# Performance work log

Measured on AMD Instinct MI355X. Metric: run time of the kernel, lower is better.

The kernel has to match this reference:

```python
import jax, jax.numpy as jnp
import numpy as np

B, N, M, D = 1, 16384, 16384, 3
CHUNK = 2048          # x tile size for the online-min KNN pass
NN_WEIGHT = 1.0       # self.nn_weight
# both_ways=False, free_weight=0, ch_normals_K=0 -> only cham_x branch is active


def setup_inputs() -> dict:
    key = jax.random.key(0)
    k1, k2, k3 = jax.random.split(key, 3)
    # LiDAR-like point clouds, scaled to a ~20 m scene extent
    pc1 = jax.random.normal(k1, (B, N, D), dtype=jnp.float32) * 10.0
    est_flow = jax.random.normal(k2, (B, N, D), dtype=jnp.float32) * 0.1
    pc2 = jax.random.normal(k3, (B, M, D), dtype=jnp.float32) * 10.0
    return {"pc1": pc1, "est_flow": est_flow, "pc2": pc2}


def _knn1_l1_dists(x, y):
    """Per-point min L1 distance from x [N,3] to y [M,3], tiled over x.

    Equivalent to knn_points(x, y, K=1, norm=1).dists[..., 0] without
    materializing the full [N, M] distance matrix.
    """
    n = x.shape[0]
    x_tiles = x.reshape(n // CHUNK, CHUNK, D)

    def tile_min(xc):  # xc: [CHUNK, 3]
        d = jnp.sum(jnp.abs(xc[:, None, :] - y[None, :, :]), axis=-1)  # [CHUNK, M]
        return jnp.min(d, axis=-1)                                     # [CHUNK]

    return jax.lax.map(tile_min, x_tiles).reshape(n)


def reference(pc1, est_flow, pc2):
    x = pc1 + est_flow                                   # deformed cloud [B,N,3]
    cham_x = jax.vmap(_knn1_l1_dists)(x, pc2)            # [B, N]
    cham_y = jnp.float32(0.0)                            # both_ways=False
    freespace_loss = jnp.zeros_like(cham_x)              # free_weight == 0 branch
    chamf_loss = NN_WEIGHT * (cham_x.mean() + cham_y)    # free_weight * 0 omitted
    return (chamf_loss, freespace_loss)
```

## Files before the change

kernel.cpp:

```cpp
#include <hip/hip_runtime.h>


#define TPB 256
#define RB 8
#define PTS_PER_BLOCK (TPB * RB)
#define YSEG 64
#define NITER (YSEG / 16)

typedef float sf16 __attribute__((ext_vector_type(16)));
typedef float sf8  __attribute__((ext_vector_type(8)));

#define SLOAD24(B16, B8, PTR, O16, O8)                                     \
  asm volatile("s_load_dwordx16 %0, %2, " O16 "\n\t"                       \
               "s_load_dwordx8  %1, %2, " O8                               \
               : "=s"(B16), "=s"(B8) : "s"(PTR));

#define SWAIT(B16, B8)                                                     \
  asm volatile("s_waitcnt lgkmcnt(0)" : "+s"(B16), "+s"(B8));

#define DIST2S(MR, AXv, AYv, AZv, Y0X, Y0Y, Y0Z, Y1X, Y1Y, Y1Z)           \
  {                                                                        \
    float t0, t1, t2, t3, t4;                                              \
    asm("v_sub_f32 %1, %9, %6\n\t"                                         \
        "v_sub_f32 %2, %10, %7\n\t"                                        \
        "v_sub_f32 %3, %11, %8\n\t"                                        \
        "v_sub_f32 %4, %12, %6\n\t"                                        \
        "v_sub_f32 %5, %13, %7\n\t"                                        \
        "v_add_f32 %1, |%1|, |%2|\n\t"                                     \
        "v_sub_f32 %2, %14, %8\n\t"                                        \
        "v_add_f32 %4, |%4|, |%5|\n\t"                                     \
        "v_add_f32 %1, %1, |%3|\n\t"                                       \
        "v_add_f32 %4, %4, |%2|\n\t"                                       \
        "v_min3_f32 %0, %0, %1, %4"                                        \
        : "+v"(MR), "=&v"(t0), "=&v"(t1), "=&v"(t2), "=&v"(t3), "=&v"(t4)  \
        : "v"(AXv), "v"(AYv), "v"(AZv),                                    \
          "s"(Y0X), "s"(Y0Y), "s"(Y0Z), "s"(Y1X), "s"(Y1Y), "s"(Y1Z));    \
  }

#define COMPUTE8(G16, G8)                                                  \
  {                                                                        \
    _Pragma("unroll")                                                      \
    for (int r = 0; r < RB; ++r)                                           \
      DIST2S(m[r], ax[r], ay[r], az[r],                                    \
             G16[0], G16[1], G16[2], G16[3], G16[4], G16[5]);              \
    _Pragma("unroll")                                                      \
    for (int r = 0; r < RB; ++r)                                           \
      DIST2S(m[r], ax[r], ay[r], az[r],                                    \
             G16[6], G16[7], G16[8], G16[9], G16[10], G16[11]);            \
    _Pragma("unroll")                                                      \
    for (int r = 0; r < RB; ++r)                                           \
      DIST2S(m[r], ax[r], ay[r], az[r],                                    \
             G16[12], G16[13], G16[14], G16[15], G8[0], G8[1]);            \
    _Pragma("unroll")                                                      \
    for (int r = 0; r < RB; ++r)                                           \
      DIST2S(m[r], ax[r], ay[r], az[r],                                    \
             G8[2], G8[3], G8[4], G8[5], G8[6], G8[7]);                    \
  }

__global__ __launch_bounds__(TPB) void init_kernel(unsigned* __restrict__ minbits, int N4) {
    const int i = blockIdx.x * TPB + threadIdx.x;
    uint4* p = (uint4*)minbits;
    if (i < N4) p[i] = make_uint4(0x7F7F7F7Fu, 0x7F7F7F7Fu, 0x7F7F7F7Fu, 0x7F7F7F7Fu);
}

__global__ __launch_bounds__(TPB, 8) void chamfer_kernel(
    const float* __restrict__ pc1, const float* __restrict__ flow,
    const float* __restrict__ pc2, unsigned* __restrict__ minbits,
    int N, int M) {
    const int t = threadIdx.x;

    const int ibase = blockIdx.x * PTS_PER_BLOCK + t;
    float ax[RB], ay[RB], az[RB];
#pragma unroll
    for (int r = 0; r < RB; ++r) {
        const int i = ibase + r * TPB;
        const int ic = (i < N) ? i : (N - 1);
        ax[r] = pc1[3 * ic]     + flow[3 * ic];
        ay[r] = pc1[3 * ic + 1] + flow[3 * ic + 1];
        az[r] = pc1[3 * ic + 2] + flow[3 * ic + 2];
    }

    float m[RB];
#pragma unroll
    for (int r = 0; r < RB; ++r) m[r] = 3.0e38f;

    const int ybase = blockIdx.y * YSEG;
    const int yend  = (ybase + YSEG < M) ? (ybase + YSEG) : M;

    if (yend - ybase == YSEG) {
        const float* yp = pc2 + (size_t)3 * (size_t)ybase;
        sf16 A16, B16; sf8 A8, B8;
        SLOAD24(A16, A8, yp, "0", "64");
#pragma unroll 1
        for (int it = 0; it < NITER; ++it) {
            SWAIT(A16, A8);
            SLOAD24(B16, B8, yp, "96", "160");
            COMPUTE8(A16, A8);
            SWAIT(B16, B8);
            if (it + 1 < NITER)
                SLOAD24(A16, A8, yp, "192", "256");
            COMPUTE8(B16, B8);
            yp += 48;
        }
    } else {
        for (int j = ybase; j < yend; ++j) {
            const float yx = pc2[3 * j], yy = pc2[3 * j + 1], yz = pc2[3 * j + 2];
#pragma unroll
            for (int r = 0; r < RB; ++r)
                m[r] = fminf(m[r], fabsf(ax[r] - yx) + fabsf(ay[r] - yy) + fabsf(az[r] - yz));
        }
    }

#pragma unroll
    for (int r = 0; r < RB; ++r) {
        const int i = ibase + r * TPB;
        if (i < N) atomicMin(&minbits[i], __float_as_uint(m[r]));
    }
}

__global__ __launch_bounds__(1024) void reduce_kernel(
    const unsigned* __restrict__ minbits, float* __restrict__ out,
    int N, int out_size) {
    float4* o4 = (float4*)out;
    const int n4 = out_size / 4;
    for (int k = threadIdx.x; k < n4; k += 1024)
        o4[k] = make_float4(0.f, 0.f, 0.f, 0.f);
    for (int k = n4 * 4 + threadIdx.x; k < out_size; k += 1024)
        out[k] = 0.f;

    float s = 0.0f;
    const uint4* p = (const uint4*)minbits;
    for (int k = threadIdx.x; k < N / 4; k += 1024) {
        uint4 v = p[k];
        s += __uint_as_float(v.x) + __uint_as_float(v.y) +
             __uint_as_float(v.z) + __uint_as_float(v.w);
    }
    for (int k = (N / 4) * 4 + threadIdx.x; k < N; k += 1024)
        s += __uint_as_float(minbits[k]);
#pragma unroll
    for (int off = 32; off > 0; off >>= 1) s += __shfl_down(s, off, 64);
    __shared__ float ls[16];
    const int wid = threadIdx.x >> 6, lane = threadIdx.x & 63;
    if (lane == 0) ls[wid] = s;
    __syncthreads();
    if (threadIdx.x == 0) {
        float tot = 0.0f;
        for (int w = 0; w < 16; ++w) tot += ls[w];
        out[0] = tot / (float)N;
    }
}

extern "C" void kernel_launch(void* const* d_in, const int* in_sizes, int n_in,
                              void* d_out, int out_size, void* d_ws, size_t ws_size,
                              hipStream_t stream) {
    const float* pc1  = (const float*)d_in[0];
    const float* flow = (const float*)d_in[1];
    const float* pc2  = (const float*)d_in[2];
    float* out = (float*)d_out;

    const int N = in_sizes[0] / 3;
    const int M = in_sizes[2] / 3;

    unsigned* minbits = (unsigned*)d_ws;

    const int nbN    = (N + PTS_PER_BLOCK - 1) / PTS_PER_BLOCK;
    const int msplit = (M + YSEG - 1) / YSEG;

    init_kernel<<<(N / 4 + TPB - 1) / TPB, TPB, 0, stream>>>(minbits, N / 4);
    chamfer_kernel<<<dim3(nbN, msplit), TPB, 0, stream>>>(pc1, flow, pc2, minbits, N, M);
    reduce_kernel<<<1, 1024, 0, stream>>>(minbits, out, N, out_size);
}
```

Measured before the change: 48.18 us.

## Retile chamfer kernel, replace init kernel with memset, parallelize output zeroing

Cuts the per-thread x-point count from 8 to 2 and lengthens each y segment from 64 to 256 points, which changes the grid shape: more blocks along x, fewer along y, so fewer atomicMin calls per output point. The init kernel is replaced by hipMemsetAsync. The single-block reduce becomes a multi-block finalize kernel, so zeroing the large freespace output is spread across blocks. With only two points per thread, each scalar-loaded y value is reused less, which may lower arithmetic intensity.

```diff
diff --git a/kernel.cpp b/kernel.cpp
--- a/kernel.cpp
+++ b/kernel.cpp
@@ -2,9 +2,9 @@
 
 
 #define TPB 256
-#define RB 8
+#define RB 2
 #define PTS_PER_BLOCK (TPB * RB)
-#define YSEG 64
+#define YSEG 256
 #define NITER (YSEG / 16)
 
 typedef float sf16 __attribute__((ext_vector_type(16)));
@@ -56,12 +56,6 @@
       DIST2S(m[r], ax[r], ay[r], az[r],                                    \
              G8[2], G8[3], G8[4], G8[5], G8[6], G8[7]);                    \
   }
-
-__global__ __launch_bounds__(TPB) void init_kernel(unsigned* __restrict__ minbits, int N4) {
-    const int i = blockIdx.x * TPB + threadIdx.x;
-    uint4* p = (uint4*)minbits;
-    if (i < N4) p[i] = make_uint4(0x7F7F7F7Fu, 0x7F7F7F7Fu, 0x7F7F7F7Fu, 0x7F7F7F7Fu);
-}
 
 __global__ __launch_bounds__(TPB, 8) void chamfer_kernel(
     const float* __restrict__ pc1, const float* __restrict__ flow,
@@ -118,35 +112,36 @@
     }
 }
 
-__global__ __launch_bounds__(1024) void reduce_kernel(
+__global__ __launch_bounds__(TPB) void finalize_kernel(
     const unsigned* __restrict__ minbits, float* __restrict__ out,
-    int N, int out_size) {
-    float4* o4 = (float4*)out;
-    const int n4 = out_size / 4;
-    for (int k = threadIdx.x; k < n4; k += 1024)
-        o4[k] = make_float4(0.f, 0.f, 0.f, 0.f);
-    for (int k = n4 * 4 + threadIdx.x; k < out_size; k += 1024)
-        out[k] = 0.f;
+    int N, int out_size, float invN) {
+    const int t = threadIdx.x;
+    const int stride = gridDim.x * TPB;
+    for (int k = blockIdx.x * TPB + t; 1 + k < out_size; k += stride)
+        out[1 + k] = 0.0f;
 
-    float s = 0.0f;
-    const uint4* p = (const uint4*)minbits;
-    for (int k = threadIdx.x; k < N / 4; k += 1024) {
-        uint4 v = p[k];
-        s += __uint_as_float(v.x) + __uint_as_float(v.y) +
-             __uint_as_float(v.z) + __uint_as_float(v.w);
-    }
-    for (int k = (N / 4) * 4 + threadIdx.x; k < N; k += 1024)
-        s += __uint_as_float(minbits[k]);
+    if (blockIdx.x == 0) {
+        float s = 0.0f;
+        const uint4* p4 = (const uint4*)minbits;
+        const int n4 = N >> 2;
+        for (int k = t; k < n4; k += TPB) {
+            uint4 v = p4[k];
+            s += __uint_as_float(v.x) + __uint_as_float(v.y) +
+                 __uint_as_float(v.z) + __uint_as_float(v.w);
+        }
+        for (int k = (n4 << 2) + t; k < N; k += TPB)
+            s += __uint_as_float(minbits[k]);
 #pragma unroll
-    for (int off = 32; off > 0; off >>= 1) s += __shfl_down(s, off, 64);
-    __shared__ float ls[16];
-    const int wid = threadIdx.x >> 6, lane = threadIdx.x & 63;
-    if (lane == 0) ls[wid] = s;
-    __syncthreads();
-    if (threadIdx.x == 0) {
-        float tot = 0.0f;
-        for (int w = 0; w < 16; ++w) tot += ls[w];
-        out[0] = tot / (float)N;
+        for (int off = 32; off > 0; off >>= 1) s += __shfl_down(s, off, 64);
+        __shared__ float ls[TPB / 64];
+        const int wid = t >> 6, lane = t & 63;
+        if (lane == 0) ls[wid] = s;
+        __syncthreads();
+        if (t == 0) {
+            float tot = 0.0f;
+            for (int w = 0; w < TPB / 64; ++w) tot += ls[w];
+            out[0] = tot * invN;
+        }
     }
 }
 
@@ -163,10 +158,12 @@
 
     unsigned* minbits = (unsigned*)d_ws;
 
+    hipMemsetAsync(minbits, 0x7F, (size_t)N * sizeof(unsigned), stream);
+
     const int nbN    = (N + PTS_PER_BLOCK - 1) / PTS_PER_BLOCK;
     const int msplit = (M + YSEG - 1) / YSEG;
+    const int nbF    = (out_size + TPB - 2) / TPB;
 
-    init_kernel<<<(N / 4 + TPB - 1) / TPB, TPB, 0, stream>>>(minbits, N / 4);
     chamfer_kernel<<<dim3(nbN, msplit), TPB, 0, stream>>>(pc1, flow, pc2, minbits, N, M);
-    reduce_kernel<<<1, 1024, 0, stream>>>(minbits, out, N, out_size);
+    finalize_kernel<<<nbF, TPB, 0, stream>>>(minbits, out, N, out_size, 1.0f / (float)N);
 }
```

New measurement: 43.91 us. -8.9%, faster.
